# Kernel tuning notes

Measured on AMD Instinct MI355X. Metric: run time of the kernel, lower is better.

The kernel has to match this reference:

```python
import jax, jax.numpy as jnp
import numpy as np

# ---- configuration matching init_kwargs ----
WINDOW = (0, 20000)
WIDTH = float(WINDOW[1] - WINDOW[0])
NBINS = (32, 64, 128)   # number of bins per binset; boundaries have nbins-1 entries
HIDDEN = 32
N_GENES = 512
N_FRAG = 2_000_000
N_MOTIF = 5_000_000


def _make_bins(nb):
    # interior boundaries of nb equal-width bins over [0, WIDTH)
    return jnp.asarray(np.linspace(0.0, WIDTH, nb + 1)[1:-1], dtype=jnp.float32)


def setup_inputs() -> dict:
    key = jax.random.key(0)
    ks = jax.random.split(key, 8)
    coordinates = jax.random.randint(ks[0], (N_FRAG,), 0, WINDOW[1], dtype=jnp.int32)
    frag_local_gene_ix = jax.random.randint(ks[1], (N_FRAG,), 0, N_GENES, dtype=jnp.int32)
    motif_positions = jax.random.randint(ks[2], (N_MOTIF,), 0, WINDOW[1], dtype=jnp.int32)
    motif_local_gene_ix = jax.random.randint(ks[3], (N_MOTIF,), 0, N_GENES, dtype=jnp.int32)
    # per-binset predictor MLP params (same shapes for every binset -> stacked)
    K = len(NBINS)
    W1 = jax.random.normal(ks[4], (K, 1, HIDDEN), dtype=jnp.float32) * 0.1
    B1 = jnp.zeros((K, HIDDEN), dtype=jnp.float32)
    W2 = jax.random.normal(ks[5], (K, HIDDEN, 1), dtype=jnp.float32) * 0.1
    B2 = jnp.zeros((K, 1), dtype=jnp.float32)
    return {
        "coordinates": coordinates,
        "frag_local_gene_ix": frag_local_gene_ix,
        "motif_positions": motif_positions,
        "motif_local_gene_ix": motif_local_gene_ix,
        "bins0": _make_bins(NBINS[0]),
        "bins1": _make_bins(NBINS[1]),
        "bins2": _make_bins(NBINS[2]),
        "W1": W1, "B1": B1, "W2": W2, "B2": B2,
    }


def reference(coordinates, frag_local_gene_ix, motif_positions,
              motif_local_gene_ix, bins0, bins1, bins2, W1, B1, W2, B2):
    coords_f = coordinates.astype(jnp.float32)          # window[0] == 0 -> already shifted
    mot_pos_f = motif_positions.astype(jnp.float32)
    lp = jnp.zeros((coordinates.shape[0],), dtype=jnp.float32)
    ones = jnp.ones((motif_positions.shape[0],), dtype=jnp.float32)
    for k, bins in enumerate((bins0, bins1, bins2)):
        nb = bins.shape[0] + 1                          # len(binset)+1 bins
        bw = bins[1] - bins[0]
        # histogram of motif hits per (gene, bin): searchsorted + bincount
        idx_m = jnp.searchsorted(bins, mot_pos_f)
        seg = motif_local_gene_ix * nb + idx_m          # local_gene_ix * (len+1) + bin
        counts = jax.ops.segment_sum(ones, seg, num_segments=N_GENES * nb) / bw
        # per-bin MLP predictor: 1 -> HIDDEN -> 1 on bincount
        h = jax.nn.relu(counts[:, None] @ W1[k] + B1[k]) @ W2[k] + B2[k]  # [G*nb, 1]
        heights = h.reshape(N_GENES, nb)                # unnormalized heights per gene
        logits = jax.nn.log_softmax(heights, axis=-1)
        # piecewise-constant density log_prob for each fragment coordinate
        idx_c = jnp.searchsorted(bins, coords_f)
        lp = lp + logits[frag_local_gene_ix, idx_c] + jnp.log(jnp.float32(nb))
    return lp - jnp.log(jnp.float32(WIDTH))
```

## Files before the change

### kernel.cpp

```cpp
#include <hip/hip_runtime.h>
#include <hip/hip_bf16.h>
#include <hip/hip_fp16.h>
#include <math.h>

#define NGENES 512
#define NB2 128
#define HIST_ELEMS (NGENES * NB2)
#define NBLK 256
#define IMG_WORDS (HIST_ELEMS / 8)
#define UNROLL 4
#define T_BYTES (HIST_ELEMS * 2)

typedef int   v4i __attribute__((ext_vector_type(4)));
typedef unsigned int v4u __attribute__((ext_vector_type(4)));
typedef float v4f __attribute__((ext_vector_type(4)));

__device__ __forceinline__ int fine_idx(int v) {
    int i = (4 * v - 1) / 625;
    i = i < 0 ? 0 : i;
    return i > 127 ? 127 : i;
}

__global__ __launch_bounds__(1024) void hist_u4_kernel(const int* __restrict__ pos,
                                                       const int* __restrict__ gene,
                                                       unsigned int* __restrict__ partial,
                                                       int nm, int chunk) {
    __shared__ unsigned int lds[IMG_WORDS];
    const int p = blockIdx.x;

    v4u* lds4 = (v4u*)lds;
    for (int i = threadIdx.x; i < IMG_WORDS / 4; i += 1024) {
        v4u z = {0u, 0u, 0u, 0u};
        lds4[i] = z;
    }
    __syncthreads();

    const int start = p * chunk;
    const int end   = min(start + chunk, nm);
    const int i4s = start >> 2;
    const int i4e = end >> 2;
    const v4i* p4 = (const v4i*)pos;
    const v4i* g4 = (const v4i*)gene;

    int base = i4s;
    for (; base + UNROLL * 1024 <= i4e; base += UNROLL * 1024) {
        v4i P[UNROLL], G[UNROLL];
#pragma unroll
        for (int k = 0; k < UNROLL; ++k) {
            const int i = base + k * 1024 + (int)threadIdx.x;
            P[k] = p4[i];
            G[k] = g4[i];
        }
#pragma unroll
        for (int k = 0; k < UNROLL; ++k) {
            int c0 = (G[k].x << 7) + fine_idx(P[k].x);
            int c1 = (G[k].y << 7) + fine_idx(P[k].y);
            int c2 = (G[k].z << 7) + fine_idx(P[k].z);
            int c3 = (G[k].w << 7) + fine_idx(P[k].w);
            atomicAdd(&lds[c0 >> 3], 1u << ((c0 & 7) << 2));
            atomicAdd(&lds[c1 >> 3], 1u << ((c1 & 7) << 2));
            atomicAdd(&lds[c2 >> 3], 1u << ((c2 & 7) << 2));
            atomicAdd(&lds[c3 >> 3], 1u << ((c3 & 7) << 2));
        }
    }
    for (int i = base + (int)threadIdx.x; i < i4e; i += 1024) {
        v4i pp = p4[i];
        v4i gg = g4[i];
        int c0 = (gg.x << 7) + fine_idx(pp.x);
        int c1 = (gg.y << 7) + fine_idx(pp.y);
        int c2 = (gg.z << 7) + fine_idx(pp.z);
        int c3 = (gg.w << 7) + fine_idx(pp.w);
        atomicAdd(&lds[c0 >> 3], 1u << ((c0 & 7) << 2));
        atomicAdd(&lds[c1 >> 3], 1u << ((c1 & 7) << 2));
        atomicAdd(&lds[c2 >> 3], 1u << ((c2 & 7) << 2));
        atomicAdd(&lds[c3 >> 3], 1u << ((c3 & 7) << 2));
    }
    for (int i = i4e * 4 + (int)threadIdx.x; i < end; i += 1024) {
        int c = (gene[i] << 7) + fine_idx(pos[i]);
        atomicAdd(&lds[c >> 3], 1u << ((c & 7) << 2));
    }
    __syncthreads();

    v4u* dst = (v4u*)(partial + (size_t)p * IMG_WORDS);
    for (int i = threadIdx.x; i < IMG_WORDS / 4; i += 1024) dst[i] = lds4[i];
}

__global__ void hist_kernel(const int* __restrict__ pos, const int* __restrict__ gene,
                            unsigned int* __restrict__ hist, int n) {
    const int tid = blockIdx.x * blockDim.x + threadIdx.x;
    const int stride = gridDim.x * blockDim.x;
    const int n4 = n >> 2;
    const v4i* p4 = (const v4i*)pos;
    const v4i* g4 = (const v4i*)gene;
    for (int i = tid; i < n4; i += stride) {
        v4i p = p4[i];
        v4i g = g4[i];
        atomicAdd(&hist[(g.x << 7) + fine_idx(p.x)], 1u);
        atomicAdd(&hist[(g.y << 7) + fine_idx(p.y)], 1u);
        atomicAdd(&hist[(g.z << 7) + fine_idx(p.z)], 1u);
        atomicAdd(&hist[(g.w << 7) + fine_idx(p.w)], 1u);
    }
    int t = n4 * 4 + tid;
    if (t < n) atomicAdd(&hist[(gene[t] << 7) + fine_idx(pos[t])], 1u);
}

__device__ __forceinline__ float mlp32(float c, const float* __restrict__ W1k,
                                       const float* __restrict__ B1k,
                                       const float* __restrict__ W2k, float b2) {
    float s = b2;
#pragma unroll
    for (int h = 0; h < 32; ++h) {
        float v = fmaf(c, W1k[h], B1k[h]);
        v = v > 0.f ? v : 0.f;
        s = fmaf(v, W2k[h], s);
    }
    return s;
}

__device__ __forceinline__ float wave_max(float v) {
#pragma unroll
    for (int off = 32; off >= 1; off >>= 1) v = fmaxf(v, __shfl_xor(v, off));
    return v;
}
__device__ __forceinline__ float wave_sum(float v) {
#pragma unroll
    for (int off = 32; off >= 1; off >>= 1) v += __shfl_xor(v, off);
    return v;
}

__device__ __forceinline__ void table_math(int g, int t, float n2a, float n2b,
                                           const float* __restrict__ W1,
                                           const float* __restrict__ B1,
                                           const float* __restrict__ W2,
                                           const float* __restrict__ B2,
                                           __half* __restrict__ T) {
    float n1 = n2a + n2b;
    float n0 = __shfl(n1, 2 * t) + __shfl(n1, 2 * t + 1);

    float h2a = mlp32(n2a / 156.25f, W1 + 64, B1 + 64, W2 + 64, B2[2]);
    float h2b = mlp32(n2b / 156.25f, W1 + 64, B1 + 64, W2 + 64, B2[2]);
    float h1  = mlp32(n1  / 312.5f,  W1 + 32, B1 + 32, W2 + 32, B2[1]);
    float h0  = mlp32(n0  / 625.0f,  W1,      B1,      W2,      B2[0]);

    float m2 = wave_max(fmaxf(h2a, h2b));
    float s2 = wave_sum(expf(h2a - m2) + expf(h2b - m2));
    float l2 = m2 + logf(s2);

    float m1 = wave_max(h1);
    float s1 = wave_sum(expf(h1 - m1));
    float l1 = m1 + logf(s1);

    float h0m = (t < 32) ? h0 : -INFINITY;
    float m0 = wave_max(h0m);
    float s0 = wave_sum((t < 32) ? expf(h0 - m0) : 0.f);
    float l0 = m0 + logf(s0);

    const float CONST = logf(32.f) + logf(64.f) + logf(128.f) - logf(20000.f);

    float ls1 = h1 - l1;
    float ls0_own = h0 - l0;
    float ls0 = __shfl(ls0_own, t >> 1);

    float base = ls1 + ls0 + CONST;
    T[(g << 7) + 2 * t]     = __float2half((h2a - l2) + base);
    T[(g << 7) + 2 * t + 1] = __float2half((h2b - l2) + base);
}

__global__ __launch_bounds__(1024) void table_from_partial(const unsigned int* __restrict__ partial,
                                                           const float* __restrict__ W1,
                                                           const float* __restrict__ B1,
                                                           const float* __restrict__ W2,
                                                           const float* __restrict__ B2,
                                                           __half* __restrict__ T) {
    const int b = blockIdx.x;
    const int t = threadIdx.x;
    __shared__ unsigned int binpair[128];
    if (t < 128) binpair[t] = 0u;
    __syncthreads();

    const int pos = t & 31;
    const int img0 = t >> 5;
    const unsigned int* src = partial + (size_t)img0 * IMG_WORDS + (b << 5) + pos;

    unsigned int ae = 0u, ao = 0u;
#pragma unroll
    for (int r = 0; r < 8; ++r) {
        unsigned int w = src[(size_t)r * 32 * IMG_WORDS];
        ae += w & 0x0F0F0F0Fu;
        ao += (w >> 4) & 0x0F0F0F0Fu;
    }
    const int gl = pos >> 4;
    const int jbase = gl * 64 + (pos & 15) * 4;
#pragma unroll
    for (int k = 0; k < 4; ++k) {
        unsigned int val = ((ae >> (8 * k)) & 0xFFu) | (((ao >> (8 * k)) & 0xFFu) << 16);
        atomicAdd(&binpair[jbase + k], val);
    }
    __syncthreads();

    if (t < 128) {
        const int j  = t >> 6;
        const int ln = t & 63;
        unsigned int v = binpair[j * 64 + ln];
        table_math(2 * b + j, ln, (float)(v & 0xFFFFu), (float)(v >> 16),
                   W1, B1, W2, B2, T);
    }
}

__global__ __launch_bounds__(64) void table_from_hist(const unsigned int* __restrict__ hist,
                                                      const float* __restrict__ W1,
                                                      const float* __restrict__ B1,
                                                      const float* __restrict__ W2,
                                                      const float* __restrict__ B2,
                                                      __half* __restrict__ T) {
    const int g = blockIdx.x;
    const int t = threadIdx.x;
    const unsigned int* hg = hist + (g << 7);
    table_math(g, t, (float)hg[2 * t], (float)hg[2 * t + 1], W1, B1, W2, B2, T);
}

__global__ __launch_bounds__(1024) void gather_lds_kernel(const int* __restrict__ coord,
                                                          const int* __restrict__ gene,
                                                          const __half* __restrict__ Th,
                                                          float* __restrict__ out, int n) {
    extern __shared__ __half Tl[];
    {
        const v4u* src = (const v4u*)Th;
        v4u* dst = (v4u*)Tl;
#pragma unroll
        for (int k = 0; k < T_BYTES / 16 / 1024; ++k)
            dst[k * 1024 + threadIdx.x] = src[k * 1024 + threadIdx.x];
    }
    __syncthreads();

    const int tid = blockIdx.x * 1024 + (int)threadIdx.x;
    const int stride = NBLK * 1024;
    const int n8 = n >> 3;
    const v4i* c4 = (const v4i*)coord;
    const v4i* g4 = (const v4i*)gene;
    v4f* o4 = (v4f*)out;
    for (int i = tid; i < n8; i += stride) {
        v4i c0 = c4[2 * i];
        v4i c1 = c4[2 * i + 1];
        v4i g0 = g4[2 * i];
        v4i g1 = g4[2 * i + 1];
        v4f oa, ob;
        oa.x = __half2float(Tl[(g0.x << 7) + fine_idx(c0.x)]);
        oa.y = __half2float(Tl[(g0.y << 7) + fine_idx(c0.y)]);
        oa.z = __half2float(Tl[(g0.z << 7) + fine_idx(c0.z)]);
        oa.w = __half2float(Tl[(g0.w << 7) + fine_idx(c0.w)]);
        ob.x = __half2float(Tl[(g1.x << 7) + fine_idx(c1.x)]);
        ob.y = __half2float(Tl[(g1.y << 7) + fine_idx(c1.y)]);
        ob.z = __half2float(Tl[(g1.z << 7) + fine_idx(c1.z)]);
        ob.w = __half2float(Tl[(g1.w << 7) + fine_idx(c1.w)]);
        o4[2 * i]     = oa;
        o4[2 * i + 1] = ob;
    }
    for (int t = n8 * 8 + tid; t < n; t += stride)
        out[t] = __half2float(Tl[(gene[t] << 7) + fine_idx(coord[t])]);
}

__global__ __launch_bounds__(256) void frag_kernel(const int* __restrict__ coord,
                                                   const int* __restrict__ gene,
                                                   const __half* __restrict__ T,
                                                   float* __restrict__ out, int n) {
    const int tid = blockIdx.x * blockDim.x + threadIdx.x;
    const int stride = gridDim.x * blockDim.x;
    const int n4 = n >> 2;
    const v4i* c4 = (const v4i*)coord;
    const v4i* g4 = (const v4i*)gene;
    v4f* o4 = (v4f*)out;
    for (int i = tid; i < n4; i += stride) {
        v4i c = c4[i];
        v4i g = g4[i];
        v4f o;
        o.x = __half2float(T[(g.x << 7) + fine_idx(c.x)]);
        o.y = __half2float(T[(g.y << 7) + fine_idx(c.y)]);
        o.z = __half2float(T[(g.z << 7) + fine_idx(c.z)]);
        o.w = __half2float(T[(g.w << 7) + fine_idx(c.w)]);
        o4[i] = o;
    }
    for (int t = n4 * 4 + tid; t < n; t += stride)
        out[t] = __half2float(T[(gene[t] << 7) + fine_idx(coord[t])]);
}

extern "C" void kernel_launch(void* const* d_in, const int* in_sizes, int n_in,
                              void* d_out, int out_size, void* d_ws, size_t ws_size,
                              hipStream_t stream) {
    const int* coords = (const int*)d_in[0];
    const int* fgene  = (const int*)d_in[1];
    const int* mpos   = (const int*)d_in[2];
    const int* mgene  = (const int*)d_in[3];
    const float* W1 = (const float*)d_in[7];
    const float* B1 = (const float*)d_in[8];
    const float* W2 = (const float*)d_in[9];
    const float* B2 = (const float*)d_in[10];

    __half* Th = (__half*)d_ws;
    unsigned int* hist = (unsigned int*)((char*)d_ws + T_BYTES);
    unsigned int* partial = (unsigned int*)((char*)d_ws + T_BYTES
                                            + HIST_ELEMS * sizeof(unsigned int));

    const int nf = in_sizes[0];
    const int nm = in_sizes[2];

    const size_t need = T_BYTES + HIST_ELEMS * sizeof(unsigned int)
                      + (size_t)NBLK * IMG_WORDS * sizeof(unsigned int);

    if (ws_size >= need) {
        int chunk = ((nm + NBLK - 1) / NBLK + 3) & ~3;
        hist_u4_kernel<<<NBLK, 1024, 0, stream>>>(mpos, mgene, partial, nm, chunk);
        table_from_partial<<<NGENES / 2, 1024, 0, stream>>>(partial, W1, B1, W2, B2, Th);
        gather_lds_kernel<<<NBLK, 1024, T_BYTES, stream>>>(coords, fgene, Th, (float*)d_out, nf);
    } else {
        (void)hipMemsetAsync(hist, 0, HIST_ELEMS * sizeof(unsigned int), stream);
        hist_kernel<<<2048, 256, 0, stream>>>(mpos, mgene, hist, nm);
        table_from_hist<<<NGENES, 64, 0, stream>>>(hist, W1, B1, W2, B2, Th);
        frag_kernel<<<1024, 256, 0, stream>>>(coords, fgene, Th, (float*)d_out, nf);
    }
}
```

Before: 27.84 us.

## Add XCD-local reduction stage for partial histograms before table build

Adds a reduce kernel of 32 blocks in which each block sums 8 partial histogram images. The images are chosen by block index modulo 8, apparently so they were written on the same XCD and are still in its local L2. The table kernel then reads 32 reduced images instead of 256 nibble-packed partials. This replaces scattered cross-XCD reads with more local ones, at the cost of an extra kernel launch and a larger workspace.

Result: slower. 32.35 us (+16.2%).

```diff
diff --git a/kernel.cpp b/kernel.cpp
--- a/kernel.cpp
+++ b/kernel.cpp
@@ -8,6 +8,8 @@
 #define HIST_ELEMS (NGENES * NB2)
 #define NBLK 256
 #define IMG_WORDS (HIST_ELEMS / 8)
+#define NRED 32
+#define RED_WORDS (HIST_ELEMS / 4)
 #define UNROLL 4
 #define T_BYTES (HIST_ELEMS * 2)
 
@@ -83,6 +85,28 @@
 
     v4u* dst = (v4u*)(partial + (size_t)p * IMG_WORDS);
     for (int i = threadIdx.x; i < IMG_WORDS / 4; i += 1024) dst[i] = lds4[i];
+}
+
+__global__ __launch_bounds__(1024) void reduce_xcd_kernel(const unsigned int* __restrict__ partial,
+                                                          unsigned int* __restrict__ red) {
+    const int j = blockIdx.x;
+    const int x = j & 7;
+    const int k = j >> 3;
+    unsigned int* dst = red + (size_t)j * RED_WORDS;
+#pragma unroll
+    for (int s = 0; s < 8; ++s) {
+        const int w = s * 1024 + (int)threadIdx.x;
+        unsigned int ae = 0u, ao = 0u;
+#pragma unroll
+        for (int i = 0; i < 8; ++i) {
+            const int b = x + 64 * k + 8 * i;
+            unsigned int v = partial[(size_t)b * IMG_WORDS + w];
+            ae += v & 0x0F0F0F0Fu;
+            ao += (v >> 4) & 0x0F0F0F0Fu;
+        }
+        dst[2 * w]     = ae;
+        dst[2 * w + 1] = ao;
+    }
 }
 
 __global__ void hist_kernel(const int* __restrict__ pos, const int* __restrict__ gene,
@@ -166,35 +190,30 @@
     T[(g << 7) + 2 * t + 1] = __float2half((h2b - l2) + base);
 }
 
-__global__ __launch_bounds__(1024) void table_from_partial(const unsigned int* __restrict__ partial,
-                                                           const float* __restrict__ W1,
-                                                           const float* __restrict__ B1,
-                                                           const float* __restrict__ W2,
-                                                           const float* __restrict__ B2,
-                                                           __half* __restrict__ T) {
+__global__ __launch_bounds__(1024) void table_from_red(const unsigned int* __restrict__ red,
+                                                       const float* __restrict__ W1,
+                                                       const float* __restrict__ B1,
+                                                       const float* __restrict__ W2,
+                                                       const float* __restrict__ B2,
+                                                       __half* __restrict__ T) {
     const int b = blockIdx.x;
     const int t = threadIdx.x;
     __shared__ unsigned int binpair[128];
     if (t < 128) binpair[t] = 0u;
     __syncthreads();
 
-    const int pos = t & 31;
-    const int img0 = t >> 5;
-    const unsigned int* src = partial + (size_t)img0 * IMG_WORDS + (b << 5) + pos;
-
-    unsigned int ae = 0u, ao = 0u;
-#pragma unroll
-    for (int r = 0; r < 8; ++r) {
-        unsigned int w = src[(size_t)r * 32 * IMG_WORDS];
-        ae += w & 0x0F0F0F0Fu;
-        ao += (w >> 4) & 0x0F0F0F0Fu;
-    }
-    const int gl = pos >> 4;
-    const int jbase = gl * 64 + (pos & 15) * 4;
-#pragma unroll
-    for (int k = 0; k < 4; ++k) {
-        unsigned int val = ((ae >> (8 * k)) & 0xFFu) | (((ao >> (8 * k)) & 0xFFu) << 16);
-        atomicAdd(&binpair[jbase + k], val);
+    const int i = t >> 5;
+    const int q = t & 31;
+    const unsigned int* src = red + (size_t)i * RED_WORDS + (b << 6) + 2 * q;
+    const unsigned int ae = src[0];
+    const unsigned int ao = src[1];
+
+    const int gl = q >> 4;
+    const int jbase = gl * 64 + (q & 15) * 4;
+#pragma unroll
+    for (int jj = 0; jj < 4; ++jj) {
+        unsigned int val = ((ae >> (8 * jj)) & 0xFFu) | (((ao >> (8 * jj)) & 0xFFu) << 16);
+        atomicAdd(&binpair[jbase + jj], val);
     }
     __syncthreads();
 
@@ -300,17 +319,22 @@
     unsigned int* hist = (unsigned int*)((char*)d_ws + T_BYTES);
     unsigned int* partial = (unsigned int*)((char*)d_ws + T_BYTES
                                             + HIST_ELEMS * sizeof(unsigned int));
+    unsigned int* red = (unsigned int*)((char*)d_ws + T_BYTES
+                                        + HIST_ELEMS * sizeof(unsigned int)
+                                        + (size_t)NBLK * IMG_WORDS * sizeof(unsigned int));
 
     const int nf = in_sizes[0];
     const int nm = in_sizes[2];
 
     const size_t need = T_BYTES + HIST_ELEMS * sizeof(unsigned int)
-                      + (size_t)NBLK * IMG_WORDS * sizeof(unsigned int);
+                      + (size_t)NBLK * IMG_WORDS * sizeof(unsigned int)
+                      + (size_t)NRED * RED_WORDS * sizeof(unsigned int);
 
     if (ws_size >= need) {
         int chunk = ((nm + NBLK - 1) / NBLK + 3) & ~3;
         hist_u4_kernel<<<NBLK, 1024, 0, stream>>>(mpos, mgene, partial, nm, chunk);
-        table_from_partial<<<NGENES / 2, 1024, 0, stream>>>(partial, W1, B1, W2, B2, Th);
+        reduce_xcd_kernel<<<NRED, 1024, 0, stream>>>(partial, red);
+        table_from_red<<<NGENES / 2, 1024, 0, stream>>>(red, W1, B1, W2, B2, Th);
         gather_lds_kernel<<<NBLK, 1024, T_BYTES, stream>>>(coords, fgene, Th, (float*)d_out, nf);
     } else {
         (void)hipMemsetAsync(hist, 0, HIST_ELEMS * sizeof(unsigned int), stream);
```
